# Kernel tuning notes

Hardware: AMD Instinct MI355X
Metric: run time of the kernel (lower is better)

## Reference

```python
import jax, jax.numpy as jnp
import numpy as np
import math

EPS = 1e-12  # matches F.normalize eps


def _l2_normalize(x):
    # F.normalize(x, p=2, dim=1): x / max(||x||, eps)
    n = jnp.sqrt(jnp.sum(x * x, axis=-1, keepdims=True))
    return x / jnp.maximum(n, EPS)


def setup_inputs() -> dict:
    key = jax.random.key(0)
    k1, k2 = jax.random.split(key)
    B, C, D = 4096, 10000, 1024
    features = jax.random.normal(k1, (B, D), dtype=jnp.float32)
    prototypes = jax.random.normal(k2, (C, D), dtype=jnp.float32)
    distance_scale = jnp.ones((1,), dtype=jnp.float32)
    temperature = jnp.ones((1,), dtype=jnp.float32)
    return {"features": features, "prototypes": prototypes,
            "distance_scale": distance_scale, "temperature": temperature}


def reference(features, prototypes, distance_scale, temperature):
    f = _l2_normalize(features)          # [B, D]
    p = _l2_normalize(prototypes)        # [C, D]
    # ||f - p||^2 = 2 - 2 f.p for unit vectors; clamp tiny negatives from fp error
    sq = jnp.maximum(2.0 - 2.0 * jnp.einsum('bd,cd->bc', f, p), EPS)
    dist = jnp.sqrt(sq) / math.sqrt(2.0)                      # [B, C]
    iso = jnp.abs(distance_scale) * dist                      # [B, C]
    logits = -(iso + jnp.mean(iso, axis=1, keepdims=True))
    return logits / temperature
```

## Files before the change

kernel.cpp:

```cpp
#include <hip/hip_runtime.h>
#include <hip/hip_bf16.h>

typedef __attribute__((ext_vector_type(8))) short short8;
typedef __attribute__((ext_vector_type(4))) float f32x4;

#define GLOBAL_AS __attribute__((address_space(1)))
#define LDS_AS    __attribute__((address_space(3)))

__device__ __forceinline__ void async_ld16(const void* g, void* l) {
    __builtin_amdgcn_global_load_lds((const GLOBAL_AS void*)g, (LDS_AS void*)l, 16, 0, 0);
}

__device__ __forceinline__ unsigned short f2bf(float x) {
    union { __hip_bfloat16 h; unsigned short u; } cv;
    cv.h = __float2bfloat16(x);
    return cv.u;
}

__global__ __launch_bounds__(256) void norm_rows_kernel(
    const float* __restrict__ in, unsigned short* __restrict__ outb, int rows_in,
    float* __restrict__ rowsum)
{
    const int row = blockIdx.x;
    const int tid = threadIdx.x;
    if (rowsum != nullptr && tid == 0) rowsum[row] = 0.f;
    float4 v = make_float4(0.f, 0.f, 0.f, 0.f);
    if (row < rows_in)
        v = reinterpret_cast<const float4*>(in + (size_t)row * 1024)[tid];
    float s = v.x * v.x + v.y * v.y + v.z * v.z + v.w * v.w;
    #pragma unroll
    for (int off = 32; off > 0; off >>= 1) s += __shfl_down(s, off);
    __shared__ float sr[4];
    if ((tid & 63) == 0) sr[tid >> 6] = s;
    __syncthreads();
    const float tot = sr[0] + sr[1] + sr[2] + sr[3];
    const float inv = 1.f / fmaxf(sqrtf(tot), 1e-12f);
    ushort4 o;
    o.x = f2bf(v.x * inv);
    o.y = f2bf(v.y * inv);
    o.z = f2bf(v.z * inv);
    o.w = f2bf(v.w * inv);
    reinterpret_cast<ushort4*>(outb + (size_t)row * 1024)[tid] = o;
}

__global__ __launch_bounds__(512, 2) void gemm_iso_kernel(
    const unsigned short* __restrict__ A,
    const unsigned short* __restrict__ B,
    float* __restrict__ out,
    float* __restrict__ rowsum,
    const float* __restrict__ ds_ptr,
    int M, int C, int K)
{
    __shared__ __align__(16) char lds[131072];

    const float dsv_raw = ds_ptr[0];

    const int tid  = threadIdx.x;
    const int lane = tid & 63;
    const int wid  = tid >> 6;

    const int orig = blockIdx.y * gridDim.x + blockIdx.x;
    const int cpx  = (gridDim.x * gridDim.y) >> 3;
    const int swz  = (orig & 7) * cpx + (orig >> 3);
    const int bx   = swz % gridDim.x;
    const int by   = swz / gridDim.x;
    const int brow = by * 256;
    const int bcol = bx * 256;

    const int lrow8 = lane >> 3;
    const int slotg = (lane & 7) ^ lrow8;
    const size_t kb = (size_t)K * 2;

    const char* pA[4]; const char* pB[4]; int lA[4], lB[4];
    #pragma unroll
    for (int i = 0; i < 4; ++i) {
        const int seg = wid * 4 + i;
        const int r   = seg * 8 + lrow8;
        pA[i] = (const char*)A + (size_t)(brow + r) * kb + slotg * 16;
        pB[i] = (const char*)B + (size_t)(bcol + r) * kb + slotg * 16;
        lA[i] = seg * 1024;
        lB[i] = 32768 + seg * 1024;
    }

    auto STAGE = [&](int buf) {
        char* base = lds + (buf << 16);
        #pragma unroll
        for (int i = 0; i < 4; ++i) async_ld16(pA[i], base + lA[i]);
        #pragma unroll
        for (int i = 0; i < 4; ++i) async_ld16(pB[i], base + lB[i]);
        #pragma unroll
        for (int i = 0; i < 4; ++i) { pA[i] += 128; pB[i] += 128; }
    };

    const int wr = (wid >> 2) * 128;
    const int wc = (wid & 3) * 64;
    const int lr = lane & 15;
    const int kq = lane >> 4;
    const int sx = lr & 7;

    f32x4 acc[8][4];
    #pragma unroll
    for (int m = 0; m < 8; ++m)
        #pragma unroll
        for (int n = 0; n < 4; ++n)
            acc[m][n] = (f32x4){0.f, 0.f, 0.f, 0.f};

    int aoff[8], boff[4];
    #pragma unroll
    for (int m = 0; m < 8; ++m) aoff[m] = (wr + m * 16 + lr) * 128;
    #pragma unroll
    for (int n = 0; n < 4; ++n) boff[n] = 32768 + (wc + n * 16 + lr) * 128;
    const int so0 = ((0 + kq) ^ sx) * 16;
    const int so1 = ((4 + kq) ^ sx) * 16;

    auto COMPUTE = [&](int buf) {
        const char* base = lds + (buf << 16);
        #pragma unroll
        for (int kk = 0; kk < 2; ++kk) {
            const int so = kk ? so1 : so0;
            short8 a[8], b[4];
            #pragma unroll
            for (int m = 0; m < 8; ++m)
                a[m] = *reinterpret_cast<const short8*>(base + aoff[m] + so);
            #pragma unroll
            for (int n = 0; n < 4; ++n)
                b[n] = *reinterpret_cast<const short8*>(base + boff[n] + so);
            __builtin_amdgcn_s_setprio(1);
            #pragma unroll
            for (int m = 0; m < 8; ++m)
                #pragma unroll
                for (int n = 0; n < 4; ++n)
                    acc[m][n] = __builtin_amdgcn_mfma_f32_16x16x32_bf16(
                        a[m], b[n], acc[m][n], 0, 0, 0);
            __builtin_amdgcn_s_setprio(0);
        }
    };

    const int nt = K >> 6;
    STAGE(0);
    asm volatile("s_waitcnt vmcnt(0)" ::: "memory");
    __builtin_amdgcn_s_barrier();
    __builtin_amdgcn_sched_barrier(0);

    for (int t = 0; t < nt; ++t) {
        if (t + 1 < nt) {
            STAGE((t + 1) & 1);
            __builtin_amdgcn_sched_barrier(0);
        }
        COMPUTE(t & 1);
        if (t + 1 < nt) {
            asm volatile("s_waitcnt vmcnt(0)" ::: "memory");
            __builtin_amdgcn_s_barrier();
            __builtin_amdgcn_sched_barrier(0);
        }
    }

    const float dsv = fabsf(dsv_raw);
    #pragma unroll
    for (int m = 0; m < 8; ++m) {
        float rs0 = 0.f, rs1 = 0.f, rs2 = 0.f, rs3 = 0.f;
        const int row0 = brow + wr + m * 16 + kq * 4;
        #pragma unroll
        for (int n = 0; n < 4; ++n) {
            const int col = bcol + wc + n * 16 + lr;
            const bool ok = col < C;
            float* op = out + (size_t)row0 * C + col;
            #pragma unroll
            for (int j = 0; j < 4; ++j) {
                const float sq  = fmaxf(2.f - 2.f * acc[m][n][j], 1e-12f);
                const float iso = dsv * (sqrtf(sq) * 0.70710678118654752f);
                if (ok) op[(size_t)j * C] = iso;
                const float c = ok ? iso : 0.f;
                if (j == 0) rs0 += c; else if (j == 1) rs1 += c;
                else if (j == 2) rs2 += c; else rs3 += c;
            }
        }
        float r4[4] = {rs0, rs1, rs2, rs3};
        #pragma unroll
        for (int j = 0; j < 4; ++j) {
            float r = r4[j];
            r += __shfl_xor(r, 1);
            r += __shfl_xor(r, 2);
            r += __shfl_xor(r, 4);
            r += __shfl_xor(r, 8);
            if (lr == 0) atomicAdd(&rowsum[row0 + j], r);
        }
    }
}

__global__ __launch_bounds__(256) void finalize_kernel(
    float* __restrict__ out, const float* __restrict__ rowsum,
    const float* __restrict__ tptr, int C)
{
    const int row = blockIdx.x;
    const float mean = rowsum[row] / (float)C;
    const float invT = 1.f / tptr[0];
    float* rp = out + (size_t)row * C;
    const int n4 = C >> 2;
    for (int i = threadIdx.x; i < n4; i += 256) {
        float4 v = reinterpret_cast<const float4*>(rp)[i];
        v.x = -(v.x + mean) * invT;
        v.y = -(v.y + mean) * invT;
        v.z = -(v.z + mean) * invT;
        v.w = -(v.w + mean) * invT;
        reinterpret_cast<float4*>(rp)[i] = v;
    }
}

extern "C" void kernel_launch(void* const* d_in, const int* in_sizes, int n_in,
                              void* d_out, int out_size, void* d_ws, size_t ws_size,
                              hipStream_t stream)
{
    const float* feat = (const float*)d_in[0];
    const float* prot = (const float*)d_in[1];
    const float* dsc  = (const float*)d_in[2];
    const float* temp = (const float*)d_in[3];
    float* out = (float*)d_out;

    const int D = 1024;
    const int M = in_sizes[0] / D;
    const int C = in_sizes[1] / D;
    const int NT = (C + 255) / 256;
    const int Npad = NT * 256;

    float* rowsum = (float*)d_ws;
    unsigned short* fbf = (unsigned short*)(rowsum + M);
    unsigned short* pbf = fbf + (size_t)M * D;

    norm_rows_kernel<<<M, 256, 0, stream>>>(feat, fbf, M, rowsum);
    norm_rows_kernel<<<Npad, 256, 0, stream>>>(prot, pbf, C, nullptr);
    gemm_iso_kernel<<<dim3(NT, M / 256), 512, 0, stream>>>(fbf, pbf, out, rowsum, dsc, M, C, D);
    finalize_kernel<<<M, 256, 0, stream>>>(out, rowsum, temp, C);
}
```

Measured before the change: 378.6 us.

## Shrink GEMM tile to 256x128 and use triple-buffered async LDS pipeline

Changes the block tile from 256x256 to 256x128 columns and the per-wave tile from 128x64 to 64x64, roughly halving accumulator registers. The LDS staging moves from double to triple buffering with a prefetch distance of two, using partial vmcnt waits so one stage of loads stays in flight during compute. The aim is more blocks in flight and better latency hiding. In exchange, reuse per loaded byte drops, since the A tile is fetched twice as often across column blocks.

New measurement: 359.2 us. 5.1% less time.

```diff
diff --git a/kernel.cpp b/kernel.cpp
--- a/kernel.cpp
+++ b/kernel.cpp
@@ -51,7 +51,7 @@
     const float* __restrict__ ds_ptr,
     int M, int C, int K)
 {
-    __shared__ __align__(16) char lds[131072];
+    __shared__ __align__(16) char lds[3 * 49152];
 
     const float dsv_raw = ds_ptr[0];
 
@@ -65,69 +65,70 @@
     const int bx   = swz % gridDim.x;
     const int by   = swz / gridDim.x;
     const int brow = by * 256;
-    const int bcol = bx * 256;
+    const int bcol = bx * 128;
 
     const int lrow8 = lane >> 3;
     const int slotg = (lane & 7) ^ lrow8;
     const size_t kb = (size_t)K * 2;
 
-    const char* pA[4]; const char* pB[4]; int lA[4], lB[4];
-    #pragma unroll
-    for (int i = 0; i < 4; ++i) {
-        const int seg = wid * 4 + i;
-        const int r   = seg * 8 + lrow8;
-        pA[i] = (const char*)A + (size_t)(brow + r) * kb + slotg * 16;
-        pB[i] = (const char*)B + (size_t)(bcol + r) * kb + slotg * 16;
-        lA[i] = seg * 1024;
-        lB[i] = 32768 + seg * 1024;
-    }
-
-    auto STAGE = [&](int buf) {
-        char* base = lds + (buf << 16);
-        #pragma unroll
-        for (int i = 0; i < 4; ++i) async_ld16(pA[i], base + lA[i]);
-        #pragma unroll
-        for (int i = 0; i < 4; ++i) async_ld16(pB[i], base + lB[i]);
-        #pragma unroll
-        for (int i = 0; i < 4; ++i) { pA[i] += 128; pB[i] += 128; }
+    const char* pG[6]; int lOff[6];
+    #pragma unroll
+    for (int i = 0; i < 6; ++i) {
+        const int seg = wid * 6 + i;
+        if (seg < 32) {
+            const int r = seg * 8 + lrow8;
+            pG[i] = (const char*)A + (size_t)(brow + r) * kb + slotg * 16;
+        } else {
+            const int r = (seg - 32) * 8 + lrow8;
+            pG[i] = (const char*)B + (size_t)(bcol + r) * kb + slotg * 16;
+        }
+        lOff[i] = seg * 1024;
+    }
+
+    auto STAGE = [&](int slot) {
+        char* base = lds + slot * 49152;
+        #pragma unroll
+        for (int i = 0; i < 6; ++i) async_ld16(pG[i], base + lOff[i]);
+        #pragma unroll
+        for (int i = 0; i < 6; ++i) pG[i] += 128;
     };
 
-    const int wr = (wid >> 2) * 128;
-    const int wc = (wid & 3) * 64;
+    const int wr = (wid >> 1) * 64;
+    const int wc = (wid & 1) * 64;
     const int lr = lane & 15;
     const int kq = lane >> 4;
     const int sx = lr & 7;
 
-    f32x4 acc[8][4];
-    #pragma unroll
-    for (int m = 0; m < 8; ++m)
+    f32x4 acc[4][4];
+    #pragma unroll
+    for (int m = 0; m < 4; ++m)
         #pragma unroll
         for (int n = 0; n < 4; ++n)
             acc[m][n] = (f32x4){0.f, 0.f, 0.f, 0.f};
 
-    int aoff[8], boff[4];
-    #pragma unroll
-    for (int m = 0; m < 8; ++m) aoff[m] = (wr + m * 16 + lr) * 128;
+    int aoff[4], boff[4];
+    #pragma unroll
+    for (int m = 0; m < 4; ++m) aoff[m] = (wr + m * 16 + lr) * 128;
     #pragma unroll
     for (int n = 0; n < 4; ++n) boff[n] = 32768 + (wc + n * 16 + lr) * 128;
     const int so0 = ((0 + kq) ^ sx) * 16;
     const int so1 = ((4 + kq) ^ sx) * 16;
 
-    auto COMPUTE = [&](int buf) {
-        const char* base = lds + (buf << 16);
+    auto COMPUTE = [&](int slot) {
+        const char* base = lds + slot * 49152;
         #pragma unroll
         for (int kk = 0; kk < 2; ++kk) {
             const int so = kk ? so1 : so0;
-            short8 a[8], b[4];
-            #pragma unroll
-            for (int m = 0; m < 8; ++m)
+            short8 a[4], b[4];
+            #pragma unroll
+            for (int m = 0; m < 4; ++m)
                 a[m] = *reinterpret_cast<const short8*>(base + aoff[m] + so);
             #pragma unroll
             for (int n = 0; n < 4; ++n)
                 b[n] = *reinterpret_cast<const short8*>(base + boff[n] + so);
             __builtin_amdgcn_s_setprio(1);
             #pragma unroll
-            for (int m = 0; m < 8; ++m)
+            for (int m = 0; m < 4; ++m)
                 #pragma unroll
                 for (int n = 0; n < 4; ++n)
                     acc[m][n] = __builtin_amdgcn_mfma_f32_16x16x32_bf16(
@@ -137,27 +138,34 @@
     };
 
     const int nt = K >> 6;
+    int slot = 0;
     STAGE(0);
-    asm volatile("s_waitcnt vmcnt(0)" ::: "memory");
+    STAGE(1);
+    asm volatile("s_waitcnt vmcnt(6)" ::: "memory");
     __builtin_amdgcn_s_barrier();
     __builtin_amdgcn_sched_barrier(0);
 
     for (int t = 0; t < nt; ++t) {
+        const bool more2 = (t + 2 < nt);
+        if (more2) {
+            STAGE((slot + 2) % 3);
+            __builtin_amdgcn_sched_barrier(0);
+        }
+        COMPUTE(slot);
         if (t + 1 < nt) {
-            STAGE((t + 1) & 1);
-            __builtin_amdgcn_sched_barrier(0);
-        }
-        COMPUTE(t & 1);
-        if (t + 1 < nt) {
-            asm volatile("s_waitcnt vmcnt(0)" ::: "memory");
+            if (more2)
+                asm volatile("s_waitcnt vmcnt(6)" ::: "memory");
+            else
+                asm volatile("s_waitcnt vmcnt(0)" ::: "memory");
             __builtin_amdgcn_s_barrier();
             __builtin_amdgcn_sched_barrier(0);
         }
+        slot = (slot + 1) % 3;
     }
 
     const float dsv = fabsf(dsv_raw);
     #pragma unroll
-    for (int m = 0; m < 8; ++m) {
+    for (int m = 0; m < 4; ++m) {
         float rs0 = 0.f, rs1 = 0.f, rs2 = 0.f, rs3 = 0.f;
         const int row0 = brow + wr + m * 16 + kq * 4;
         #pragma unroll
@@ -220,8 +228,8 @@
     const int D = 1024;
     const int M = in_sizes[0] / D;
     const int C = in_sizes[1] / D;
-    const int NT = (C + 255) / 256;
-    const int Npad = NT * 256;
+    const int NT = (C + 127) / 128;
+    const int Npad = NT * 128;
 
     float* rowsum = (float*)d_ws;
     unsigned short* fbf = (unsigned short*)(rowsum + M);
```
